# Optimization experiments

Measured on AMD Instinct MI355X. Metric: run time of the kernel, lower is better.

Reference implementation:

```python
import jax, jax.numpy as jnp
import numpy as np

# Static config (must match init_kwargs)
IMG_H, IMG_W = 48, 160
BEV_H, BEV_W = 128, 128
X_MIN, X_MAX, Y_MIN, Y_MAX = -51.2, 51.2, -51.2, 51.2
RES_X = (X_MAX - X_MIN) / BEV_W
RES_Y = (Y_MAX - Y_MIN) / BEV_H
C, D, B = 128, 64, 2


def setup_inputs() -> dict:
    key = jax.random.key(0)
    k1, k2, k3, k4 = jax.random.split(key, 4)
    img_features = jax.random.normal(k1, (B, C, IMG_H, IMG_W), dtype=jnp.float32)
    # depth distribution per pixel (softmax over D, as a depth net would emit)
    depth_probs = jax.nn.softmax(jax.random.normal(k2, (B, D, IMG_H, IMG_W), dtype=jnp.float32), axis=1)
    # depth bin centers: 1m .. 60m
    depth_values = jnp.linspace(1.0, 60.0, D, dtype=jnp.float32)
    # realistic pinhole intrinsics (feature-map scale) with tiny per-cam jitter
    fx, fy, cx, cy = 120.0, 120.0, IMG_W / 2.0, IMG_H / 2.0
    K0 = jnp.array([[fx, 0.0, cx], [0.0, fy, cy], [0.0, 0.0, 1.0]], dtype=jnp.float32)
    K = K0[None] + 0.01 * jax.random.normal(k3, (B, 3, 3), dtype=jnp.float32) * jnp.array(
        [[1.0, 0.0, 1.0], [0.0, 1.0, 1.0], [0.0, 0.0, 0.0]], dtype=jnp.float32)
    # cam->lidar extrinsic: cam z (forward) -> lidar x, cam x -> -lidar y, cam y -> -lidar z
    R0 = jnp.array([[0.0, 0.0, 1.0], [-1.0, 0.0, 0.0], [0.0, -1.0, 0.0]], dtype=jnp.float32)
    t0 = jnp.array([1.5, 0.0, 1.8], dtype=jnp.float32)
    T0 = jnp.eye(4, dtype=jnp.float32).at[:3, :3].set(R0).at[:3, 3].set(t0)
    T = T0[None] + jnp.zeros((B, 4, 4), dtype=jnp.float32)
    T = T.at[:, :3, 3].add(0.05 * jax.random.normal(k4, (B, 3), dtype=jnp.float32))
    return {"img_features": img_features, "depth_probs": depth_probs,
            "depth_values": depth_values, "K": K, "T": T}


def _lss_forward(img_features, depth_probs, depth_values, K, T):
    Bn, Cn, H, W = img_features.shape
    Dn = depth_values.shape[0]
    # homogeneous pixel grid [H, W, 3]
    gx, gy = jnp.meshgrid(jnp.arange(W, dtype=jnp.float32),
                          jnp.arange(H, dtype=jnp.float32), indexing="xy")
    grid = jnp.stack([gx, gy, jnp.ones_like(gx)], axis=-1)
    # unproject: rays [B, H, W, 3]
    K_inv = jnp.linalg.inv(K)
    rays = jnp.einsum("bij,hwj->bhwi", K_inv, grid)
    # points in camera frame [B, D, H, W, 3]
    pts_cam = depth_values[None, :, None, None, None] * rays[:, None]
    # camera -> lidar
    pts = jnp.einsum("bij,bdhwj->bdhwi", T[:, :3, :3], pts_cam) + T[:, None, None, None, :3, 3]
    x, y, z = pts[..., 0], pts[..., 1], pts[..., 2]
    # torch .long() truncates toward zero -> astype int32 matches
    bx = ((x - X_MIN) / RES_X).astype(jnp.int32)
    by = ((y - Y_MIN) / RES_Y).astype(jnp.int32)
    valid = (bx >= 0) & (bx < BEV_W) & (by >= 0) & (by < BEV_H) & (z > 0)
    # depth-weighted features [B, D, H, W, C], masked instead of gathered
    weighted = jnp.einsum("bchw,bdhw->bdhwc", img_features, depth_probs)
    weighted = weighted * valid[..., None]
    idx = jnp.where(valid, by * BEV_W + bx, 0).reshape(Bn, -1)
    feats = weighted.reshape(Bn, -1, Cn)
    bev_flat = jax.vmap(lambda f, i: jax.ops.segment_sum(f, i, num_segments=BEV_H * BEV_W))(feats, idx)
    return bev_flat.reshape(Bn, BEV_H, BEV_W, Cn).transpose(0, 3, 1, 2)


def reference(img_features, depth_probs, depth_values, K, T):
    return _lss_forward(img_features, depth_probs, depth_values, K, T)
```

## Files before the change

### kernel.cpp

```cpp
#include <hip/hip_runtime.h>

constexpr int IMG_H = 48, IMG_W = 160;
constexpr int HW    = IMG_H * IMG_W;
constexpr int BEV_H = 128, BEV_W = 128;
constexpr int NCELL = BEV_H * BEV_W;
constexpr int C_DIM = 128, D_DIM = 64, B_DIM = 2;
constexpr int NCELL_TOT = B_DIM * NCELL;
constexpr int NPIX_TOT  = B_DIM * HW;
constexpr int NPTS      = NPIX_TOT * D_DIM;
constexpr int MAX_ENTRIES = NPTS;
constexpr int CHUNK = 64;
constexpr int WAVES_PER_BLK = 4;
constexpr int NSHARD = 16;
constexpr int CNT_BLOCKS = NPTS / 256;
constexpr int TRN_BLOCKS = (HW / 32) * (C_DIM / 32) * B_DIM;
constexpr float X_MIN = -51.2f, Y_MIN = -51.2f;
constexpr float RES_X = 102.4f / 128.0f;
constexpr float RES_Y = 102.4f / 128.0f;

typedef _Float16 half2v __attribute__((ext_vector_type(2)));

constexpr size_t WS_IMG_T = 0;
constexpr size_t WS_IMG_T_WORDS = (size_t)B_DIM * HW * C_DIM / 2;
constexpr size_t WS_HIST2 = WS_IMG_T + WS_IMG_T_WORDS;
constexpr size_t WS_OUT_T = WS_HIST2 + (size_t)NSHARD * NCELL_TOT;
constexpr size_t WS_HIST  = WS_OUT_T + (size_t)NCELL_TOT * C_DIM;
constexpr size_t WS_OFFS  = WS_HIST + NCELL_TOT;
constexpr size_t WS_EKEY  = WS_OFFS + NCELL_TOT + 4;
constexpr size_t WS_EW16  = WS_EKEY + MAX_ENTRIES;
constexpr size_t WS_NEED_CM = (WS_EW16 + MAX_ENTRIES / 2) * 4;

__device__ inline int point_shard(int tid) {
    return ((tid >> 2) + (tid >> 8)) & (NSHARD - 1);
}

__device__ inline void make_ray(const float* __restrict__ K, int b, float gx, float gy,
                                float& rx, float& ry, float& rz) {
    const float* Kb = K + b * 9;
    const float a00 = Kb[0], a01 = Kb[1], a02 = Kb[2];
    const float a10 = Kb[3], a11 = Kb[4], a12 = Kb[5];
    const float a20 = Kb[6], a21 = Kb[7], a22 = Kb[8];
    const float det = a00 * (a11 * a22 - a12 * a21)
                    - a01 * (a10 * a22 - a12 * a20)
                    + a02 * (a10 * a21 - a11 * a20);
    const float inv = 1.0f / det;
    const float i00 =  (a11 * a22 - a12 * a21) * inv;
    const float i01 = -(a01 * a22 - a02 * a21) * inv;
    const float i02 =  (a01 * a12 - a02 * a11) * inv;
    const float i10 = -(a10 * a22 - a12 * a20) * inv;
    const float i11 =  (a00 * a22 - a02 * a20) * inv;
    const float i12 = -(a00 * a12 - a02 * a10) * inv;
    const float i20 =  (a10 * a21 - a11 * a20) * inv;
    const float i21 = -(a00 * a21 - a01 * a20) * inv;
    const float i22 =  (a00 * a11 - a01 * a10) * inv;
    rx = i00 * gx + i01 * gy + i02;
    ry = i10 * gx + i11 * gy + i12;
    rz = i20 * gx + i21 * gy + i22;
}

__device__ inline int point_gcell(int tid, const float* __restrict__ dv,
                                  const float* __restrict__ K,
                                  const float* __restrict__ T) {
    const int pix = tid % HW;
    const int bd  = tid / HW;
    const int d   = bd % D_DIM;
    const int b   = bd / D_DIM;
    const int h = pix / IMG_W, w = pix % IMG_W;
    float rx, ry, rz;
    make_ray(K, b, (float)w, (float)h, rx, ry, rz);
    const float* Tb = T + b * 16;
    const float dep = dv[d];
    const float px = dep * rx, py = dep * ry, pz = dep * rz;
    const float x = Tb[0] * px + Tb[1] * py + Tb[2]  * pz + Tb[3];
    const float y = Tb[4] * px + Tb[5] * py + Tb[6]  * pz + Tb[7];
    const float z = Tb[8] * px + Tb[9] * py + Tb[10] * pz + Tb[11];
    const int bx = (int)((x - X_MIN) / RES_X);
    const int by = (int)((y - Y_MIN) / RES_Y);
    const bool valid = (bx >= 0) && (bx < BEV_W) && (by >= 0) && (by < BEV_H) && (z > 0.0f);
    return valid ? (b * NCELL + by * BEV_W + bx) : -1;
}

__device__ inline bool wave_runs(int gcell, int lane, int& run_len, int& leader_idx) {
    const int left = __shfl_up(gcell, 1);
    const bool is_leader = (lane == 0) || (left != gcell);
    const unsigned long long lmask = __ballot(is_leader);
    const unsigned long long rest = (lane == 63) ? 0ULL : (lmask >> (lane + 1));
    const int f = __ffsll((unsigned long long)rest);
    run_len = f ? f : (64 - lane);
    const unsigned long long below =
        lmask & ((lane == 63) ? ~0ULL : ((1ULL << (lane + 1)) - 1ULL));
    leader_idx = 63 - __clzll((long long)below);
    return is_leader;
}

__global__ __launch_bounds__(256) void k_prep(const float* __restrict__ img,
                                              _Float16* __restrict__ img_t,
                                              const float* __restrict__ dv,
                                              const float* __restrict__ K,
                                              const float* __restrict__ T,
                                              int* __restrict__ hist2) {
    __shared__ float tile[32][33];
    if (blockIdx.x < CNT_BLOCKS) {
        const int tid = blockIdx.x * 256 + threadIdx.x;
        const int gcell = point_gcell(tid, dv, K, T);
        const int lane = threadIdx.x & 63;
        int run_len, leader_idx;
        const bool lead = wave_runs(gcell, lane, run_len, leader_idx);
        if (lead && gcell >= 0)
            atomicAdd(&hist2[(size_t)point_shard(tid) * NCELL_TOT + gcell], run_len);
    } else {
        const int bi = blockIdx.x - CNT_BLOCKS;
        const int px_t = bi % (HW / 32);
        const int c_t  = (bi / (HW / 32)) % (C_DIM / 32);
        const int b    = bi / ((HW / 32) * (C_DIM / 32));
        const int tx = threadIdx.x & 31, ty = threadIdx.x >> 5;
        const int pix0 = px_t * 32, c0 = c_t * 32;
        #pragma unroll
        for (int j = 0; j < 32; j += 8)
            tile[ty + j][tx] = img[((size_t)(b * C_DIM + c0 + ty + j)) * HW + pix0 + tx];
        __syncthreads();
        #pragma unroll
        for (int j = 0; j < 32; j += 8)
            img_t[((size_t)(b * HW + pix0 + ty + j)) * C_DIM + c0 + tx] =
                (_Float16)tile[tx][ty + j];
    }
}

__global__ __launch_bounds__(256) void k_reduce(const int* __restrict__ hist2,
                                                int* __restrict__ hist) {
    const int cell = blockIdx.x * 256 + threadIdx.x;
    int s = 0;
    #pragma unroll
    for (int sh = 0; sh < NSHARD; ++sh)
        s += hist2[(size_t)sh * NCELL_TOT + cell];
    hist[cell] = s;
}

__global__ __launch_bounds__(1024) void k_scan(const int* __restrict__ hist,
                                               int* __restrict__ offs) {
    __shared__ int lds[1024];
    const int t = threadIdx.x;
    int h[32];
    int s = 0;
    const int base = t * 32;
    #pragma unroll
    for (int k = 0; k < 32; ++k) { h[k] = hist[base + k]; s += h[k]; }
    lds[t] = s;
    __syncthreads();
    for (int off = 1; off < 1024; off <<= 1) {
        int v = (t >= off) ? lds[t - off] : 0;
        __syncthreads();
        lds[t] += v;
        __syncthreads();
    }
    int run = lds[t] - s;
    #pragma unroll
    for (int k = 0; k < 32; ++k) {
        offs[base + k] = run;
        run += h[k];
    }
    if (t == 1023) offs[NCELL_TOT] = lds[1023];
}

__global__ __launch_bounds__(256) void k_shardbase(int* __restrict__ hist2,
                                                   const int* __restrict__ offs) {
    const int cell = blockIdx.x * 256 + threadIdx.x;
    int run = offs[cell];
    #pragma unroll
    for (int sh = 0; sh < NSHARD; ++sh) {
        const size_t idx = (size_t)sh * NCELL_TOT + cell;
        const int cnt = hist2[idx];
        hist2[idx] = run;
        run += cnt;
    }
}

__global__ __launch_bounds__(256) void k_fill(const float* __restrict__ dp,
                                              const float* __restrict__ dv,
                                              const float* __restrict__ K,
                                              const float* __restrict__ T,
                                              int* __restrict__ cursor2,
                                              int* __restrict__ ekey,
                                              unsigned short* __restrict__ ew16) {
    const int tid = blockIdx.x * 256 + threadIdx.x;
    const int gcell = point_gcell(tid, dv, K, T);
    const int lane = threadIdx.x & 63;
    int run_len, leader_idx;
    const bool lead = wave_runs(gcell, lane, run_len, leader_idx);
    int base = 0;
    if (lead && gcell >= 0)
        base = atomicAdd(&cursor2[(size_t)point_shard(tid) * NCELL_TOT + gcell], run_len);
    base = __shfl(base, leader_idx);
    if (gcell < 0) return;
    const int slot = base + (lane - leader_idx);
    const float p = dp[tid];
    ekey[slot] = (gcell << 13) | (tid % HW);
    ew16[slot] = (unsigned short)__float2uint_rn(p * 65535.0f);
}

template <bool CELL_MAJOR>
__global__ __launch_bounds__(256) void k_chunk_gather(
    const _Float16* __restrict__ img_t,
    const int* __restrict__ offs,
    const int* __restrict__ ekey,
    const unsigned short* __restrict__ ew16,
    float* __restrict__ acc_out)
{
    const int total = offs[NCELL_TOT];
    const int wave  = threadIdx.x >> 6;
    const int lane  = threadIdx.x & 63;
    const int base  = (blockIdx.x * WAVES_PER_BLK + wave) * CHUNK;
    if (base >= total) return;

    const int eidx = min(base + lane, total - 1);
    const int   mykey = ekey[eidx];
    const float myw   = (base + lane < total)
                        ? (float)ew16[base + lane] * (1.0f / 65535.0f) : 0.0f;
    const int mywi = __float_as_int(myw);

    const int c2 = lane * 2;
    int prev = __builtin_amdgcn_readlane(mykey, 0) >> 13;
    float2 acc = make_float2(0.0f, 0.0f);

#define LOADG(g, V)                                                              \
    do {                                                                         \
        _Pragma("unroll")                                                        \
        for (int k = 0; k < 8; ++k) {                                            \
            const int key = __builtin_amdgcn_readlane(mykey, (g) * 8 + k);       \
            const int pix = key & 8191;                                          \
            const int bb  = key >> 27;                                           \
            V[k] = *reinterpret_cast<const half2v*>(                             \
                &img_t[((size_t)(bb * HW + pix)) * C_DIM + c2]);                 \
        }                                                                        \
    } while (0)

#define FLUSHP(cell)                                                             \
    do {                                                                         \
        if (CELL_MAJOR) {                                                        \
            float* o = &acc_out[(size_t)(cell) * C_DIM + c2];                    \
            atomicAdd(o, acc.x);                                                 \
            atomicAdd(o + 1, acc.y);                                             \
        } else {                                                                 \
            const int pb = (cell) >> 14, pc = (cell) & (NCELL - 1);              \
            float* o = &acc_out[((size_t)(pb * C_DIM + c2)) * NCELL + pc];       \
            atomicAdd(o, acc.x);                                                 \
            atomicAdd(o + NCELL, acc.y);                                         \
        }                                                                        \
    } while (0)

#define ACCG(g, V)                                                               \
    do {                                                                         \
        _Pragma("unroll")                                                        \
        for (int k = 0; k < 8; ++k) {                                            \
            const int   key = __builtin_amdgcn_readlane(mykey, (g) * 8 + k);     \
            const float wgt =                                                    \
                __int_as_float(__builtin_amdgcn_readlane(mywi, (g) * 8 + k));    \
            const int gcell = key >> 13;                                         \
            if (gcell != prev) {                              \
                FLUSHP(prev);                                                    \
                acc = make_float2(0.0f, 0.0f);                                   \
                prev = gcell;                                                    \
            }                                                                    \
            acc.x = fmaf((float)V[k][0], wgt, acc.x);                            \
            acc.y = fmaf((float)V[k][1], wgt, acc.y);                            \
        }                                                                        \
    } while (0)

    half2v va[8], vb[8];
    LOADG(0, va);
    LOADG(1, vb);
    ACCG(0, va);
    LOADG(2, va);
    ACCG(1, vb);
    LOADG(3, vb);
    ACCG(2, va);
    LOADG(4, va);
    ACCG(3, vb);
    LOADG(5, vb);
    ACCG(4, va);
    LOADG(6, va);
    ACCG(5, vb);
    LOADG(7, vb);
    ACCG(6, va);
    ACCG(7, vb);
    FLUSHP(prev);

#undef LOADG
#undef FLUSHP
#undef ACCG
}

__global__ __launch_bounds__(256) void k_untranspose(const float* __restrict__ out_t,
                                                     float* __restrict__ out) {
    __shared__ float tile[32][33];
    const int b = blockIdx.z;
    const int tx = threadIdx.x, ty = threadIdx.y;
    const int cell0 = blockIdx.x * 32, c0 = blockIdx.y * 32;
    const float* src = out_t + (size_t)b * NCELL * C_DIM;
    #pragma unroll
    for (int j = 0; j < 32; j += 8)
        tile[ty + j][tx] = src[((size_t)(cell0 + ty + j)) * C_DIM + c0 + tx];
    __syncthreads();
    #pragma unroll
    for (int j = 0; j < 32; j += 8)
        out[((size_t)(b * C_DIM + c0 + ty + j)) * NCELL + cell0 + tx] = tile[tx][ty + j];
}

extern "C" void kernel_launch(void* const* d_in, const int* in_sizes, int n_in,
                              void* d_out, int out_size, void* d_ws, size_t ws_size,
                              hipStream_t stream) {
    const float* img = (const float*)d_in[0];
    const float* dp  = (const float*)d_in[1];
    const float* dv  = (const float*)d_in[2];
    const float* K   = (const float*)d_in[3];
    const float* T   = (const float*)d_in[4];
    float* out = (float*)d_out;

    float* ws_f   = (float*)d_ws;
    _Float16* img_t = (_Float16*)d_ws;
    int*   hist2  = (int*)d_ws + WS_HIST2;
    float* out_t  = ws_f + WS_OUT_T;
    int*   hist   = (int*)d_ws + WS_HIST;
    int*   offs   = (int*)d_ws + WS_OFFS;
    int*   ekey   = (int*)d_ws + WS_EKEY;
    unsigned short* ew16 = (unsigned short*)((int*)d_ws + WS_EW16);

    const bool cell_major = (ws_size >= WS_NEED_CM);

    if (cell_major) {
        hipMemsetAsync(hist2, 0,
                       ((size_t)NSHARD * NCELL_TOT + (size_t)NCELL_TOT * C_DIM) * sizeof(int),
                       stream);
    } else {
        hipMemsetAsync(hist2, 0, (size_t)NSHARD * NCELL_TOT * sizeof(int), stream);
        hipMemsetAsync(out, 0, (size_t)out_size * sizeof(float), stream);
    }

    k_prep<<<CNT_BLOCKS + TRN_BLOCKS, 256, 0, stream>>>(img, img_t, dv, K, T, hist2);
    k_reduce<<<NCELL_TOT / 256, 256, 0, stream>>>(hist2, hist);
    k_scan<<<1, 1024, 0, stream>>>(hist, offs);
    k_shardbase<<<NCELL_TOT / 256, 256, 0, stream>>>(hist2, offs);
    k_fill<<<NPTS / 256, 256, 0, stream>>>(dp, dv, K, T, hist2, ekey, ew16);
    constexpr int GATHER_BLOCKS = MAX_ENTRIES / (CHUNK * WAVES_PER_BLK);
    if (cell_major) {
        k_chunk_gather<true><<<GATHER_BLOCKS, 256, 0, stream>>>(
            img_t, offs, ekey, ew16, out_t);
        k_untranspose<<<dim3(NCELL / 32, C_DIM / 32, B_DIM), dim3(32, 8), 0, stream>>>(
            out_t, out);
    } else {
        k_chunk_gather<false><<<GATHER_BLOCKS, 256, 0, stream>>>(
            img_t, offs, ekey, ew16, out);
    }
}
```

Baseline: 147.9 us.

## Fuse all pipeline stages into one persistent kernel with grid barriers

Replaces the seven-kernel pipeline (prep, reduce, scan, shardbase, fill, gather, untranspose) with a single persistent kernel of 512 blocks. The stages are separated by software grid-wide barriers built on agent-scope atomics. The single-block scan becomes a two-level block scan, and the shard reduction is merged with the shard-base pass. The aim is to remove launch gaps and the serial single-block scan. In exchange it relies on all 512 blocks being co-resident (two per CU via launch bounds), adds spin-wait barrier overhead, drops the row-major fallback, and ignores ws_size.

```diff
diff --git a/kernel.cpp b/kernel.cpp
--- a/kernel.cpp
+++ b/kernel.cpp
@@ -10,10 +10,11 @@
 constexpr int NPTS      = NPIX_TOT * D_DIM;
 constexpr int MAX_ENTRIES = NPTS;
 constexpr int CHUNK = 64;
-constexpr int WAVES_PER_BLK = 4;
 constexpr int NSHARD = 16;
+constexpr int G     = 512;
 constexpr int CNT_BLOCKS = NPTS / 256;
 constexpr int TRN_BLOCKS = (HW / 32) * (C_DIM / 32) * B_DIM;
+constexpr int UNT_TILES  = (NCELL / 32) * (C_DIM / 32) * B_DIM;
 constexpr float X_MIN = -51.2f, Y_MIN = -51.2f;
 constexpr float RES_X = 102.4f / 128.0f;
 constexpr float RES_Y = 102.4f / 128.0f;
@@ -21,14 +22,15 @@
 typedef _Float16 half2v __attribute__((ext_vector_type(2)));
 
 constexpr size_t WS_IMG_T = 0;
-constexpr size_t WS_IMG_T_WORDS = (size_t)B_DIM * HW * C_DIM / 2;
-constexpr size_t WS_HIST2 = WS_IMG_T + WS_IMG_T_WORDS;
+constexpr size_t WS_BAR   = WS_IMG_T + (size_t)B_DIM * HW * C_DIM / 2;
+constexpr size_t WS_HIST2 = WS_BAR + 4;
 constexpr size_t WS_OUT_T = WS_HIST2 + (size_t)NSHARD * NCELL_TOT;
 constexpr size_t WS_HIST  = WS_OUT_T + (size_t)NCELL_TOT * C_DIM;
 constexpr size_t WS_OFFS  = WS_HIST + NCELL_TOT;
-constexpr size_t WS_EKEY  = WS_OFFS + NCELL_TOT + 4;
+constexpr size_t WS_BSUM  = WS_OFFS + NCELL_TOT + 4;
+constexpr size_t WS_EKEY  = WS_BSUM + 128;
 constexpr size_t WS_EW16  = WS_EKEY + MAX_ENTRIES;
-constexpr size_t WS_NEED_CM = (WS_EW16 + MAX_ENTRIES / 2) * 4;
+constexpr size_t MEMSET_WORDS = 4 + (size_t)NSHARD * NCELL_TOT + (size_t)NCELL_TOT * C_DIM;
 
 __device__ inline int point_shard(int tid) {
     return ((tid >> 2) + (tid >> 8)) & (NSHARD - 1);
@@ -93,134 +95,148 @@
     return is_leader;
 }
 
-__global__ __launch_bounds__(256) void k_prep(const float* __restrict__ img,
-                                              _Float16* __restrict__ img_t,
-                                              const float* __restrict__ dv,
-                                              const float* __restrict__ K,
-                                              const float* __restrict__ T,
-                                              int* __restrict__ hist2) {
+__device__ inline void gsync(int* __restrict__ bar, int epoch) {
+    __syncthreads();
+    if (threadIdx.x == 0) {
+        __threadfence();
+        if (__hip_atomic_fetch_add(&bar[0], 1, __ATOMIC_ACQ_REL,
+                                   __HIP_MEMORY_SCOPE_AGENT) == G - 1) {
+            __hip_atomic_store(&bar[0], 0, __ATOMIC_RELAXED, __HIP_MEMORY_SCOPE_AGENT);
+            __hip_atomic_store(&bar[1], epoch, __ATOMIC_RELEASE, __HIP_MEMORY_SCOPE_AGENT);
+        } else {
+            while (__hip_atomic_load(&bar[1], __ATOMIC_ACQUIRE,
+                                     __HIP_MEMORY_SCOPE_AGENT) < epoch)
+                __builtin_amdgcn_s_sleep(4);
+        }
+    }
+    __syncthreads();
+}
+
+__global__ __launch_bounds__(256, 2) void k_mega(
+    const float* __restrict__ img, const float* __restrict__ dp,
+    const float* __restrict__ dv, const float* __restrict__ K,
+    const float* __restrict__ T,
+    _Float16* __restrict__ img_t, int* __restrict__ bar,
+    int* __restrict__ hist2, float* __restrict__ out_t,
+    int* __restrict__ hist, int* __restrict__ offs, int* __restrict__ bsum,
+    int* __restrict__ ekey, unsigned short* __restrict__ ew16,
+    float* __restrict__ out)
+{
     __shared__ float tile[32][33];
-    if (blockIdx.x < CNT_BLOCKS) {
-        const int tid = blockIdx.x * 256 + threadIdx.x;
+    __shared__ int ldsi[256];
+    const int t = threadIdx.x;
+    const int lane = t & 63;
+    const int wave = t >> 6;
+
+    for (int u = blockIdx.x; u < CNT_BLOCKS + TRN_BLOCKS; u += G) {
+        if (u < CNT_BLOCKS) {
+            const int tid = u * 256 + t;
+            const int gcell = point_gcell(tid, dv, K, T);
+            int run_len, leader_idx;
+            const bool lead = wave_runs(gcell, lane, run_len, leader_idx);
+            if (lead && gcell >= 0)
+                atomicAdd(&hist2[(size_t)point_shard(tid) * NCELL_TOT + gcell], run_len);
+        } else {
+            const int bi = u - CNT_BLOCKS;
+            const int px_t = bi % (HW / 32);
+            const int c_t  = (bi / (HW / 32)) % (C_DIM / 32);
+            const int b    = bi / ((HW / 32) * (C_DIM / 32));
+            const int tx = t & 31, ty = t >> 5;
+            const int pix0 = px_t * 32, c0 = c_t * 32;
+            __syncthreads();
+            #pragma unroll
+            for (int j = 0; j < 32; j += 8)
+                tile[ty + j][tx] = img[((size_t)(b * C_DIM + c0 + ty + j)) * HW + pix0 + tx];
+            __syncthreads();
+            #pragma unroll
+            for (int j = 0; j < 32; j += 8)
+                img_t[((size_t)(b * HW + pix0 + ty + j)) * C_DIM + c0 + tx] =
+                    (_Float16)tile[tx][ty + j];
+        }
+    }
+    gsync(bar, 1);
+
+    for (int cell = blockIdx.x * 256 + t; cell < NCELL_TOT; cell += G * 256) {
+        int run = 0;
+        #pragma unroll
+        for (int sh = 0; sh < NSHARD; ++sh) {
+            const size_t idx = (size_t)sh * NCELL_TOT + cell;
+            const int c = hist2[idx];
+            hist2[idx] = run;
+            run += c;
+        }
+        hist[cell] = run;
+    }
+    gsync(bar, 2);
+
+    if (blockIdx.x < NCELL_TOT / 256) {
+        const int cell = blockIdx.x * 256 + t;
+        const int h = hist[cell];
+        ldsi[t] = h;
+        __syncthreads();
+        #pragma unroll
+        for (int off = 1; off < 256; off <<= 1) {
+            const int v = (t >= off) ? ldsi[t - off] : 0;
+            __syncthreads();
+            ldsi[t] += v;
+            __syncthreads();
+        }
+        offs[cell] = ldsi[t] - h;
+        if (t == 255) bsum[blockIdx.x] = ldsi[255];
+    }
+    gsync(bar, 3);
+
+    if (blockIdx.x == 0) {
+        const int v = (t < 128) ? bsum[t] : 0;
+        ldsi[t] = v;
+        __syncthreads();
+        #pragma unroll
+        for (int off = 1; off < 256; off <<= 1) {
+            const int u2 = (t >= off) ? ldsi[t - off] : 0;
+            __syncthreads();
+            ldsi[t] += u2;
+            __syncthreads();
+        }
+        if (t < 128) bsum[t] = ldsi[t] - v;
+        if (t == 127) offs[NCELL_TOT] = ldsi[127];
+    }
+    gsync(bar, 4);
+
+    if (blockIdx.x < NCELL_TOT / 256)
+        offs[blockIdx.x * 256 + t] += bsum[blockIdx.x];
+    gsync(bar, 5);
+
+    for (int tid = blockIdx.x * 256 + t; tid < NPTS; tid += G * 256) {
         const int gcell = point_gcell(tid, dv, K, T);
-        const int lane = threadIdx.x & 63;
         int run_len, leader_idx;
         const bool lead = wave_runs(gcell, lane, run_len, leader_idx);
+        int base = 0;
         if (lead && gcell >= 0)
-            atomicAdd(&hist2[(size_t)point_shard(tid) * NCELL_TOT + gcell], run_len);
-    } else {
-        const int bi = blockIdx.x - CNT_BLOCKS;
-        const int px_t = bi % (HW / 32);
-        const int c_t  = (bi / (HW / 32)) % (C_DIM / 32);
-        const int b    = bi / ((HW / 32) * (C_DIM / 32));
-        const int tx = threadIdx.x & 31, ty = threadIdx.x >> 5;
-        const int pix0 = px_t * 32, c0 = c_t * 32;
-        #pragma unroll
-        for (int j = 0; j < 32; j += 8)
-            tile[ty + j][tx] = img[((size_t)(b * C_DIM + c0 + ty + j)) * HW + pix0 + tx];
-        __syncthreads();
-        #pragma unroll
-        for (int j = 0; j < 32; j += 8)
-            img_t[((size_t)(b * HW + pix0 + ty + j)) * C_DIM + c0 + tx] =
-                (_Float16)tile[tx][ty + j];
-    }
-}
-
-__global__ __launch_bounds__(256) void k_reduce(const int* __restrict__ hist2,
-                                                int* __restrict__ hist) {
-    const int cell = blockIdx.x * 256 + threadIdx.x;
-    int s = 0;
-    #pragma unroll
-    for (int sh = 0; sh < NSHARD; ++sh)
-        s += hist2[(size_t)sh * NCELL_TOT + cell];
-    hist[cell] = s;
-}
-
-__global__ __launch_bounds__(1024) void k_scan(const int* __restrict__ hist,
-                                               int* __restrict__ offs) {
-    __shared__ int lds[1024];
-    const int t = threadIdx.x;
-    int h[32];
-    int s = 0;
-    const int base = t * 32;
-    #pragma unroll
-    for (int k = 0; k < 32; ++k) { h[k] = hist[base + k]; s += h[k]; }
-    lds[t] = s;
-    __syncthreads();
-    for (int off = 1; off < 1024; off <<= 1) {
-        int v = (t >= off) ? lds[t - off] : 0;
-        __syncthreads();
-        lds[t] += v;
-        __syncthreads();
-    }
-    int run = lds[t] - s;
-    #pragma unroll
-    for (int k = 0; k < 32; ++k) {
-        offs[base + k] = run;
-        run += h[k];
-    }
-    if (t == 1023) offs[NCELL_TOT] = lds[1023];
-}
-
-__global__ __launch_bounds__(256) void k_shardbase(int* __restrict__ hist2,
-                                                   const int* __restrict__ offs) {
-    const int cell = blockIdx.x * 256 + threadIdx.x;
-    int run = offs[cell];
-    #pragma unroll
-    for (int sh = 0; sh < NSHARD; ++sh) {
-        const size_t idx = (size_t)sh * NCELL_TOT + cell;
-        const int cnt = hist2[idx];
-        hist2[idx] = run;
-        run += cnt;
-    }
-}
-
-__global__ __launch_bounds__(256) void k_fill(const float* __restrict__ dp,
-                                              const float* __restrict__ dv,
-                                              const float* __restrict__ K,
-                                              const float* __restrict__ T,
-                                              int* __restrict__ cursor2,
-                                              int* __restrict__ ekey,
-                                              unsigned short* __restrict__ ew16) {
-    const int tid = blockIdx.x * 256 + threadIdx.x;
-    const int gcell = point_gcell(tid, dv, K, T);
-    const int lane = threadIdx.x & 63;
-    int run_len, leader_idx;
-    const bool lead = wave_runs(gcell, lane, run_len, leader_idx);
-    int base = 0;
-    if (lead && gcell >= 0)
-        base = atomicAdd(&cursor2[(size_t)point_shard(tid) * NCELL_TOT + gcell], run_len);
-    base = __shfl(base, leader_idx);
-    if (gcell < 0) return;
-    const int slot = base + (lane - leader_idx);
-    const float p = dp[tid];
-    ekey[slot] = (gcell << 13) | (tid % HW);
-    ew16[slot] = (unsigned short)__float2uint_rn(p * 65535.0f);
-}
-
-template <bool CELL_MAJOR>
-__global__ __launch_bounds__(256) void k_chunk_gather(
-    const _Float16* __restrict__ img_t,
-    const int* __restrict__ offs,
-    const int* __restrict__ ekey,
-    const unsigned short* __restrict__ ew16,
-    float* __restrict__ acc_out)
-{
-    const int total = offs[NCELL_TOT];
-    const int wave  = threadIdx.x >> 6;
-    const int lane  = threadIdx.x & 63;
-    const int base  = (blockIdx.x * WAVES_PER_BLK + wave) * CHUNK;
-    if (base >= total) return;
-
-    const int eidx = min(base + lane, total - 1);
-    const int   mykey = ekey[eidx];
-    const float myw   = (base + lane < total)
-                        ? (float)ew16[base + lane] * (1.0f / 65535.0f) : 0.0f;
-    const int mywi = __float_as_int(myw);
-
-    const int c2 = lane * 2;
-    int prev = __builtin_amdgcn_readlane(mykey, 0) >> 13;
-    float2 acc = make_float2(0.0f, 0.0f);
+            base = offs[gcell]
+                 + atomicAdd(&hist2[(size_t)point_shard(tid) * NCELL_TOT + gcell], run_len);
+        base = __shfl(base, leader_idx);
+        if (gcell >= 0) {
+            const int slot = base + (lane - leader_idx);
+            const float p = dp[tid];
+            ekey[slot] = (gcell << 13) | (tid % HW);
+            ew16[slot] = (unsigned short)__float2uint_rn(p * 65535.0f);
+        }
+    }
+    gsync(bar, 6);
+
+    {
+        const int total = offs[NCELL_TOT];
+        const int nch = (total + CHUNK - 1) >> 6;
+        for (int ci = blockIdx.x * 4 + wave; ci < nch; ci += G * 4) {
+            const int base = ci * CHUNK;
+            const int eidx = min(base + lane, total - 1);
+            const int   mykey = ekey[eidx];
+            const float myw   = (base + lane < total)
+                                ? (float)ew16[base + lane] * (1.0f / 65535.0f) : 0.0f;
+            const int mywi = __float_as_int(myw);
+            const int c2 = lane * 2;
+            int prev = __builtin_amdgcn_readlane(mykey, 0) >> 13;
+            float2 acc = make_float2(0.0f, 0.0f);
 
 #define LOADG(g, V)                                                              \
     do {                                                                         \
@@ -236,16 +252,9 @@
 
 #define FLUSHP(cell)                                                             \
     do {                                                                         \
-        if (CELL_MAJOR) {                                                        \
-            float* o = &acc_out[(size_t)(cell) * C_DIM + c2];                    \
-            atomicAdd(o, acc.x);                                                 \
-            atomicAdd(o + 1, acc.y);                                             \
-        } else {                                                                 \
-            const int pb = (cell) >> 14, pc = (cell) & (NCELL - 1);              \
-            float* o = &acc_out[((size_t)(pb * C_DIM + c2)) * NCELL + pc];       \
-            atomicAdd(o, acc.x);                                                 \
-            atomicAdd(o + NCELL, acc.y);                                         \
-        }                                                                        \
+        float* o = &out_t[(size_t)(cell) * C_DIM + c2];                          \
+        atomicAdd(o, acc.x);                                                     \
+        atomicAdd(o + 1, acc.y);                                                 \
     } while (0)
 
 #define ACCG(g, V)                                                               \
@@ -256,7 +265,7 @@
             const float wgt =                                                    \
                 __int_as_float(__builtin_amdgcn_readlane(mywi, (g) * 8 + k));    \
             const int gcell = key >> 13;                                         \
-            if (gcell != prev) {                              \
+            if (gcell != prev) {                                                 \
                 FLUSHP(prev);                                                    \
                 acc = make_float2(0.0f, 0.0f);                                   \
                 prev = gcell;                                                    \
@@ -266,44 +275,47 @@
         }                                                                        \
     } while (0)
 
-    half2v va[8], vb[8];
-    LOADG(0, va);
-    LOADG(1, vb);
-    ACCG(0, va);
-    LOADG(2, va);
-    ACCG(1, vb);
-    LOADG(3, vb);
-    ACCG(2, va);
-    LOADG(4, va);
-    ACCG(3, vb);
-    LOADG(5, vb);
-    ACCG(4, va);
-    LOADG(6, va);
-    ACCG(5, vb);
-    LOADG(7, vb);
-    ACCG(6, va);
-    ACCG(7, vb);
-    FLUSHP(prev);
-
+            half2v va[8], vb[8];
+            LOADG(0, va);
+            LOADG(1, vb);
+            ACCG(0, va);
+            LOADG(2, va);
+            ACCG(1, vb);
+            LOADG(3, vb);
+            ACCG(2, va);
+            LOADG(4, va);
+            ACCG(3, vb);
+            LOADG(5, vb);
+            ACCG(4, va);
+            LOADG(6, va);
+            ACCG(5, vb);
+            LOADG(7, vb);
+            ACCG(6, va);
+            ACCG(7, vb);
+            FLUSHP(prev);
 #undef LOADG
 #undef FLUSHP
 #undef ACCG
-}
-
-__global__ __launch_bounds__(256) void k_untranspose(const float* __restrict__ out_t,
-                                                     float* __restrict__ out) {
-    __shared__ float tile[32][33];
-    const int b = blockIdx.z;
-    const int tx = threadIdx.x, ty = threadIdx.y;
-    const int cell0 = blockIdx.x * 32, c0 = blockIdx.y * 32;
-    const float* src = out_t + (size_t)b * NCELL * C_DIM;
-    #pragma unroll
-    for (int j = 0; j < 32; j += 8)
-        tile[ty + j][tx] = src[((size_t)(cell0 + ty + j)) * C_DIM + c0 + tx];
-    __syncthreads();
-    #pragma unroll
-    for (int j = 0; j < 32; j += 8)
-        out[((size_t)(b * C_DIM + c0 + ty + j)) * NCELL + cell0 + tx] = tile[tx][ty + j];
+        }
+    }
+    gsync(bar, 7);
+
+    for (int u = blockIdx.x; u < UNT_TILES; u += G) {
+        const int cell_t = u % (NCELL / 32);
+        const int c_t    = (u / (NCELL / 32)) % (C_DIM / 32);
+        const int b      = u / ((NCELL / 32) * (C_DIM / 32));
+        const int tx = t & 31, ty = t >> 5;
+        const int cell0 = cell_t * 32, c0 = c_t * 32;
+        const float* src = out_t + (size_t)b * NCELL * C_DIM;
+        __syncthreads();
+        #pragma unroll
+        for (int j = 0; j < 32; j += 8)
+            tile[ty + j][tx] = src[((size_t)(cell0 + ty + j)) * C_DIM + c0 + tx];
+        __syncthreads();
+        #pragma unroll
+        for (int j = 0; j < 32; j += 8)
+            out[((size_t)(b * C_DIM + c0 + ty + j)) * NCELL + cell0 + tx] = tile[tx][ty + j];
+    }
 }
 
 extern "C" void kernel_launch(void* const* d_in, const int* in_sizes, int n_in,
@@ -316,39 +328,19 @@
     const float* T   = (const float*)d_in[4];
     float* out = (float*)d_out;
 
-    float* ws_f   = (float*)d_ws;
     _Float16* img_t = (_Float16*)d_ws;
+    int*   bar    = (int*)d_ws + WS_BAR;
     int*   hist2  = (int*)d_ws + WS_HIST2;
-    float* out_t  = ws_f + WS_OUT_T;
+    float* out_t  = (float*)d_ws + WS_OUT_T;
     int*   hist   = (int*)d_ws + WS_HIST;
     int*   offs   = (int*)d_ws + WS_OFFS;
+    int*   bsum   = (int*)d_ws + WS_BSUM;
     int*   ekey   = (int*)d_ws + WS_EKEY;
     unsigned short* ew16 = (unsigned short*)((int*)d_ws + WS_EW16);
-
-    const bool cell_major = (ws_size >= WS_NEED_CM);
-
-    if (cell_major) {
-        hipMemsetAsync(hist2, 0,
-                       ((size_t)NSHARD * NCELL_TOT + (size_t)NCELL_TOT * C_DIM) * sizeof(int),
-                       stream);
-    } else {
-        hipMemsetAsync(hist2, 0, (size_t)NSHARD * NCELL_TOT * sizeof(int), stream);
-        hipMemsetAsync(out, 0, (size_t)out_size * sizeof(float), stream);
-    }
-
-    k_prep<<<CNT_BLOCKS + TRN_BLOCKS, 256, 0, stream>>>(img, img_t, dv, K, T, hist2);
-    k_reduce<<<NCELL_TOT / 256, 256, 0, stream>>>(hist2, hist);
-    k_scan<<<1, 1024, 0, stream>>>(hist, offs);
-    k_shardbase<<<NCELL_TOT / 256, 256, 0, stream>>>(hist2, offs);
-    k_fill<<<NPTS / 256, 256, 0, stream>>>(dp, dv, K, T, hist2, ekey, ew16);
-    constexpr int GATHER_BLOCKS = MAX_ENTRIES / (CHUNK * WAVES_PER_BLK);
-    if (cell_major) {
-        k_chunk_gather<true><<<GATHER_BLOCKS, 256, 0, stream>>>(
-            img_t, offs, ekey, ew16, out_t);
-        k_untranspose<<<dim3(NCELL / 32, C_DIM / 32, B_DIM), dim3(32, 8), 0, stream>>>(
-            out_t, out);
-    } else {
-        k_chunk_gather<false><<<GATHER_BLOCKS, 256, 0, stream>>>(
-            img_t, offs, ekey, ew16, out);
-    }
-}
+    (void)ws_size;
+
+    hipMemsetAsync(bar, 0, MEMSET_WORDS * sizeof(int), stream);
+
+    k_mega<<<G, 256, 0, stream>>>(img, dp, dv, K, T, img_t, bar, hist2, out_t,
+                                  hist, offs, bsum, ekey, ew16, out);
+}
```

New measurement: 539.0 us. +264.5%, slower.

## Fuse reduce/scan/shardbase into decoupled-lookback scan and skip atomics for interior cells

Applied to the files above, without the earlier changes.

Replaces three kernels (shard reduce, single-block scan, shard base) with one multi-block scan that uses a decoupled look-back over per-block flags, storing shard-relative cursors that k_fill adds to the cell offset. In the gather, cells that do not span chunk boundaries are written with plain stores instead of atomics, and only cells shared with neighbouring chunks use atomicAdd. It also drops the non-cell-major fallback path. The goal is to cut launches, the serial single-block scan, and atomic traffic. In exchange it relies on spin-waiting between blocks, which assumes forward progress of earlier blocks.

```diff
diff --git a/kernel.cpp b/kernel.cpp
--- a/kernel.cpp
+++ b/kernel.cpp
@@ -14,6 +14,7 @@
 constexpr int NSHARD = 16;
 constexpr int CNT_BLOCKS = NPTS / 256;
 constexpr int TRN_BLOCKS = (HW / 32) * (C_DIM / 32) * B_DIM;
+constexpr int SCAN_BLOCKS = NCELL_TOT / 256;
 constexpr float X_MIN = -51.2f, Y_MIN = -51.2f;
 constexpr float RES_X = 102.4f / 128.0f;
 constexpr float RES_Y = 102.4f / 128.0f;
@@ -21,14 +22,13 @@
 typedef _Float16 half2v __attribute__((ext_vector_type(2)));
 
 constexpr size_t WS_IMG_T = 0;
-constexpr size_t WS_IMG_T_WORDS = (size_t)B_DIM * HW * C_DIM / 2;
-constexpr size_t WS_HIST2 = WS_IMG_T + WS_IMG_T_WORDS;
+constexpr size_t WS_FLAGS = WS_IMG_T + (size_t)B_DIM * HW * C_DIM / 2;
+constexpr size_t WS_HIST2 = WS_FLAGS + 128;
 constexpr size_t WS_OUT_T = WS_HIST2 + (size_t)NSHARD * NCELL_TOT;
-constexpr size_t WS_HIST  = WS_OUT_T + (size_t)NCELL_TOT * C_DIM;
-constexpr size_t WS_OFFS  = WS_HIST + NCELL_TOT;
+constexpr size_t WS_OFFS  = WS_OUT_T + (size_t)NCELL_TOT * C_DIM;
 constexpr size_t WS_EKEY  = WS_OFFS + NCELL_TOT + 4;
 constexpr size_t WS_EW16  = WS_EKEY + MAX_ENTRIES;
-constexpr size_t WS_NEED_CM = (WS_EW16 + MAX_ENTRIES / 2) * 4;
+constexpr size_t MEMSET_WORDS = 128 + (size_t)NSHARD * NCELL_TOT + (size_t)NCELL_TOT * C_DIM;
 
 __device__ inline int point_shard(int tid) {
     return ((tid >> 2) + (tid >> 8)) & (NSHARD - 1);
@@ -126,59 +126,81 @@
     }
 }
 
-__global__ __launch_bounds__(256) void k_reduce(const int* __restrict__ hist2,
-                                                int* __restrict__ hist) {
-    const int cell = blockIdx.x * 256 + threadIdx.x;
-    int s = 0;
+__global__ __launch_bounds__(256) void k_scan_fused(int* __restrict__ hist2,
+                                                    int* __restrict__ offs,
+                                                    unsigned* __restrict__ flags) {
+    __shared__ int lds[256];
+    __shared__ int s_base;
+    const int b = blockIdx.x;
+    const int t = threadIdx.x;
+    const int cell = b * 256 + t;
+    int run = 0;
     #pragma unroll
-    for (int sh = 0; sh < NSHARD; ++sh)
-        s += hist2[(size_t)sh * NCELL_TOT + cell];
-    hist[cell] = s;
-}
-
-__global__ __launch_bounds__(1024) void k_scan(const int* __restrict__ hist,
-                                               int* __restrict__ offs) {
-    __shared__ int lds[1024];
-    const int t = threadIdx.x;
-    int h[32];
-    int s = 0;
-    const int base = t * 32;
+    for (int sh = 0; sh < NSHARD; ++sh) {
+        const size_t idx = (size_t)sh * NCELL_TOT + cell;
+        const int c = hist2[idx];
+        hist2[idx] = run;
+        run += c;
+    }
+    const int h = run;
+    lds[t] = h;
+    __syncthreads();
     #pragma unroll
-    for (int k = 0; k < 32; ++k) { h[k] = hist[base + k]; s += h[k]; }
-    lds[t] = s;
-    __syncthreads();
-    for (int off = 1; off < 1024; off <<= 1) {
-        int v = (t >= off) ? lds[t - off] : 0;
+    for (int off = 1; off < 256; off <<= 1) {
+        const int v = (t >= off) ? lds[t - off] : 0;
         __syncthreads();
         lds[t] += v;
         __syncthreads();
     }
-    int run = lds[t] - s;
-    #pragma unroll
-    for (int k = 0; k < 32; ++k) {
-        offs[base + k] = run;
-        run += h[k];
-    }
-    if (t == 1023) offs[NCELL_TOT] = lds[1023];
-}
-
-__global__ __launch_bounds__(256) void k_shardbase(int* __restrict__ hist2,
-                                                   const int* __restrict__ offs) {
-    const int cell = blockIdx.x * 256 + threadIdx.x;
-    int run = offs[cell];
-    #pragma unroll
-    for (int sh = 0; sh < NSHARD; ++sh) {
-        const size_t idx = (size_t)sh * NCELL_TOT + cell;
-        const int cnt = hist2[idx];
-        hist2[idx] = run;
-        run += cnt;
-    }
+    const int incl = lds[t];
+    const int S = lds[255];
+    if (t == 0) {
+        const unsigned w = (((b == 0) ? 2u : 1u) << 30) | (unsigned)S;
+        __hip_atomic_store(&flags[b], w, __ATOMIC_RELEASE, __HIP_MEMORY_SCOPE_AGENT);
+        if (b == 0) s_base = 0;
+    }
+    if (b > 0 && t < 64) {
+        int sum = 0;
+        int p = b - 1;
+        bool done = false;
+        while (!done) {
+            const int idx = p - t;
+            unsigned w;
+            if (idx >= 0) {
+                do {
+                    w = __hip_atomic_load(&flags[idx], __ATOMIC_ACQUIRE,
+                                          __HIP_MEMORY_SCOPE_AGENT);
+                } while ((w >> 30) == 0);
+            } else {
+                w = 2u << 30;
+            }
+            const unsigned long long m2 = __ballot((w >> 30) == 2u);
+            const int first2 = __ffsll(m2) - 1;
+            const int limit = (first2 < 0) ? 63 : first2;
+            int contrib = (t <= limit && idx >= 0) ? (int)(w & 0x3FFFFFFFu) : 0;
+            #pragma unroll
+            for (int o = 32; o > 0; o >>= 1) contrib += __shfl_down(contrib, o);
+            sum += __shfl(contrib, 0);
+            if (first2 >= 0) done = true;
+            else p -= 64;
+        }
+        if (t == 0) {
+            s_base = sum;
+            const unsigned w2 = (2u << 30) | (unsigned)(sum + S);
+            __hip_atomic_store(&flags[b], w2, __ATOMIC_RELEASE, __HIP_MEMORY_SCOPE_AGENT);
+        }
+    }
+    __syncthreads();
+    const int base = s_base;
+    offs[cell] = base + incl - h;
+    if (cell == NCELL_TOT - 1) offs[NCELL_TOT] = base + S;
 }
 
 __global__ __launch_bounds__(256) void k_fill(const float* __restrict__ dp,
                                               const float* __restrict__ dv,
                                               const float* __restrict__ K,
                                               const float* __restrict__ T,
+                                              const int* __restrict__ offs,
                                               int* __restrict__ cursor2,
                                               int* __restrict__ ekey,
                                               unsigned short* __restrict__ ew16) {
@@ -189,7 +211,8 @@
     const bool lead = wave_runs(gcell, lane, run_len, leader_idx);
     int base = 0;
     if (lead && gcell >= 0)
-        base = atomicAdd(&cursor2[(size_t)point_shard(tid) * NCELL_TOT + gcell], run_len);
+        base = offs[gcell]
+             + atomicAdd(&cursor2[(size_t)point_shard(tid) * NCELL_TOT + gcell], run_len);
     base = __shfl(base, leader_idx);
     if (gcell < 0) return;
     const int slot = base + (lane - leader_idx);
@@ -198,13 +221,12 @@
     ew16[slot] = (unsigned short)__float2uint_rn(p * 65535.0f);
 }
 
-template <bool CELL_MAJOR>
 __global__ __launch_bounds__(256) void k_chunk_gather(
     const _Float16* __restrict__ img_t,
     const int* __restrict__ offs,
     const int* __restrict__ ekey,
     const unsigned short* __restrict__ ew16,
-    float* __restrict__ acc_out)
+    float* __restrict__ out_t)
 {
     const int total = offs[NCELL_TOT];
     const int wave  = threadIdx.x >> 6;
@@ -219,7 +241,12 @@
     const int mywi = __float_as_int(myw);
 
     const int c2 = lane * 2;
-    int prev = __builtin_amdgcn_readlane(mykey, 0) >> 13;
+    const int fc    = __builtin_amdgcn_readlane(mykey, 0) >> 13;
+    const int lcell = __builtin_amdgcn_readlane(mykey, 63) >> 13;
+    const bool shared_first = (base > 0) && ((ekey[base - 1] >> 13) == fc);
+    const bool shared_last  = (base + CHUNK < total) && ((ekey[base + CHUNK] >> 13) == lcell);
+
+    int prev = fc;
     float2 acc = make_float2(0.0f, 0.0f);
 
 #define LOADG(g, V)                                                              \
@@ -236,15 +263,14 @@
 
 #define FLUSHP(cell)                                                             \
     do {                                                                         \
-        if (CELL_MAJOR) {                                                        \
-            float* o = &acc_out[(size_t)(cell) * C_DIM + c2];                    \
+        float* o = &out_t[(size_t)(cell) * C_DIM + c2];                          \
+        const bool shared_ = ((cell) == fc && shared_first) ||                   \
+                             ((cell) == lcell && shared_last);                   \
+        if (shared_) {                                                           \
             atomicAdd(o, acc.x);                                                 \
             atomicAdd(o + 1, acc.y);                                             \
         } else {                                                                 \
-            const int pb = (cell) >> 14, pc = (cell) & (NCELL - 1);              \
-            float* o = &acc_out[((size_t)(pb * C_DIM + c2)) * NCELL + pc];       \
-            atomicAdd(o, acc.x);                                                 \
-            atomicAdd(o + NCELL, acc.y);                                         \
+            *reinterpret_cast<float2*>(o) = acc;            \
         }                                                                        \
     } while (0)
 
@@ -316,39 +342,22 @@
     const float* T   = (const float*)d_in[4];
     float* out = (float*)d_out;
 
-    float* ws_f   = (float*)d_ws;
     _Float16* img_t = (_Float16*)d_ws;
+    unsigned* flags = (unsigned*)((int*)d_ws + WS_FLAGS);
     int*   hist2  = (int*)d_ws + WS_HIST2;
-    float* out_t  = ws_f + WS_OUT_T;
-    int*   hist   = (int*)d_ws + WS_HIST;
+    float* out_t  = (float*)d_ws + WS_OUT_T;
     int*   offs   = (int*)d_ws + WS_OFFS;
     int*   ekey   = (int*)d_ws + WS_EKEY;
     unsigned short* ew16 = (unsigned short*)((int*)d_ws + WS_EW16);
-
-    const bool cell_major = (ws_size >= WS_NEED_CM);
-
-    if (cell_major) {
-        hipMemsetAsync(hist2, 0,
-                       ((size_t)NSHARD * NCELL_TOT + (size_t)NCELL_TOT * C_DIM) * sizeof(int),
-                       stream);
-    } else {
-        hipMemsetAsync(hist2, 0, (size_t)NSHARD * NCELL_TOT * sizeof(int), stream);
-        hipMemsetAsync(out, 0, (size_t)out_size * sizeof(float), stream);
-    }
+    (void)ws_size;
+
+    hipMemsetAsync(flags, 0, MEMSET_WORDS * sizeof(int), stream);
 
     k_prep<<<CNT_BLOCKS + TRN_BLOCKS, 256, 0, stream>>>(img, img_t, dv, K, T, hist2);
-    k_reduce<<<NCELL_TOT / 256, 256, 0, stream>>>(hist2, hist);
-    k_scan<<<1, 1024, 0, stream>>>(hist, offs);
-    k_shardbase<<<NCELL_TOT / 256, 256, 0, stream>>>(hist2, offs);
-    k_fill<<<NPTS / 256, 256, 0, stream>>>(dp, dv, K, T, hist2, ekey, ew16);
+    k_scan_fused<<<SCAN_BLOCKS, 256, 0, stream>>>(hist2, offs, flags);
+    k_fill<<<NPTS / 256, 256, 0, stream>>>(dp, dv, K, T, offs, hist2, ekey, ew16);
     constexpr int GATHER_BLOCKS = MAX_ENTRIES / (CHUNK * WAVES_PER_BLK);
-    if (cell_major) {
-        k_chunk_gather<true><<<GATHER_BLOCKS, 256, 0, stream>>>(
-            img_t, offs, ekey, ew16, out_t);
-        k_untranspose<<<dim3(NCELL / 32, C_DIM / 32, B_DIM), dim3(32, 8), 0, stream>>>(
-            out_t, out);
-    } else {
-        k_chunk_gather<false><<<GATHER_BLOCKS, 256, 0, stream>>>(
-            img_t, offs, ekey, ew16, out);
-    }
-}
+    k_chunk_gather<<<GATHER_BLOCKS, 256, 0, stream>>>(img_t, offs, ekey, ew16, out_t);
+    k_untranspose<<<dim3(NCELL / 32, C_DIM / 32, B_DIM), dim3(32, 8), 0, stream>>>(
+        out_t, out);
+}
```

Result: faster. 140.7 us (-4.8%).
